# Kernel tuning notes

Measured on AMD Instinct MI355X. Metric: run time of the kernel, lower is better.

## Reference

```python
import jax, jax.numpy as jnp
import numpy as np

N_NODES = 50000
N_EDGES = 800000
F_DIM = 128   # float_feat_dim
H_DIM = 64    # hidden_dim
NEG_SLOPE = 0.2


def setup_inputs() -> dict:
    key = jax.random.key(0)
    ks = jax.random.split(key, 12)
    in_dim = F_DIM + 1
    sc_in = 1.0 / np.sqrt(in_dim)
    sc_h = 1.0 / np.sqrt(H_DIM)
    return {
        "x_float": jax.random.normal(ks[0], (N_NODES, F_DIM), dtype=jnp.float32),
        "x_binary": jax.random.uniform(ks[1], (N_NODES,), dtype=jnp.float32),
        "edge_index": jax.random.randint(ks[2], (2, N_EDGES), 0, N_NODES, dtype=jnp.int64),
        "Wl": jax.random.normal(ks[3], (H_DIM, in_dim), dtype=jnp.float32) * sc_in,
        "bl": jnp.zeros((H_DIM,), dtype=jnp.float32),
        "Wr": jax.random.normal(ks[4], (H_DIM, in_dim), dtype=jnp.float32) * sc_in,
        "br": jnp.zeros((H_DIM,), dtype=jnp.float32),
        "att": jax.random.normal(ks[5], (H_DIM,), dtype=jnp.float32) * sc_h,
        "gat_bias": jnp.zeros((H_DIM,), dtype=jnp.float32),
        "Wo": jax.random.normal(ks[6], (F_DIM, H_DIM), dtype=jnp.float32) * sc_h,
        "bo": jnp.zeros((F_DIM,), dtype=jnp.float32),
        "dispersion": jnp.zeros((F_DIM,), dtype=jnp.float32),
    }


def reference(x_float, x_binary, edge_index, Wl, bl, Wr, br, att, gat_bias, Wo, bo, dispersion):
    N = x_float.shape[0]
    # concat float feats with binary feature -> [N, F+1]
    x = jnp.concatenate([x_float, x_binary[:, None]], axis=1)
    # add self loops (PyG GATv2Conv default)
    loops = jnp.arange(N, dtype=edge_index.dtype)
    src = jnp.concatenate([edge_index[0], loops])  # [E+N]
    dst = jnp.concatenate([edge_index[1], loops])
    # separate source/target linear projections (share_weights=False)
    xl = x @ Wl.T + bl  # [N, H]
    xr = x @ Wr.T + br  # [N, H]
    # per-edge GATv2 attention score: a^T LeakyReLU(x_l[j] + x_r[i])
    m = xl[src] + xr[dst]                      # [E+N, H]
    m = jnp.where(m > 0, m, NEG_SLOPE * m)
    e = m @ att                                # [E+N]
    # segment softmax over destination neighborhoods
    emax = jax.ops.segment_max(e, dst, num_segments=N)  # self loops => every seg nonempty
    ex = jnp.exp(e - emax[dst])
    denom = jax.ops.segment_sum(ex, dst, num_segments=N)
    alpha = ex / denom[dst]                    # [E+N]
    # weighted scatter-aggregate of source projections
    out = jax.ops.segment_sum(alpha[:, None] * xl[src], dst, num_segments=N) + gat_bias
    h = jax.nn.elu(out)                        # [N, H]
    logits = h @ Wo.T + bo                     # [N, F]
    return logits, jax.nn.softplus(dispersion)
```

## Files before the change

kernel.cpp:

```cpp
#include <hip/hip_runtime.h>
#include <hip/hip_bf16.h>
#include <math.h>

#define N_NODES 50000
#define N_EDGES 800000
#define F_DIM 128
#define H_DIM 64
#define IN_DIM 129
#define ETOT (N_EDGES + N_NODES)
#define PROJ_BLKS ((N_NODES + 31) / 32)
#define NB 196
#define CAP 6144
#define EPB 3125
#define BKT_BLKS 256
#define AGG_BLKS 3125

typedef __hip_bfloat16 bf16;
typedef __attribute__((ext_vector_type(8))) short bf16x8;
typedef __attribute__((ext_vector_type(4))) float f32x4;

static __device__ __forceinline__ float bs2f(short s) {
    union { float f; unsigned u; } c; c.u = ((unsigned)(unsigned short)s) << 16; return c.f;
}
static __device__ __forceinline__ short f2bs(float f) {
    union { bf16 b; short s; } u; u.b = __float2bfloat16(f); return u.s;
}

__global__ __launch_bounds__(256) void prep_kernel(
    const float* __restrict__ Wl, const float* __restrict__ Wr,
    const float* __restrict__ Wo,
    bf16* __restrict__ whi, bf16* __restrict__ wlo,
    bf16* __restrict__ wohi, bf16* __restrict__ wolo,
    int* __restrict__ gtot)
{
    int b = blockIdx.x, t = threadIdx.x;
    if (b < 8) {
        int s = b * 256 + t;
        int fid = s >> 6, l = s & 63;
        int wave = fid >> 3, nt = (fid >> 2) & 1, ks = fid & 3;
        int ch = wave * 32 + nt * 16 + (l & 15);
        int kb = ks * 32 + (l >> 4) * 8;
        const float* wrow = (ch < 64) ? Wl + (size_t)ch * IN_DIM
                                      : Wr + (size_t)(ch - 64) * IN_DIM;
        #pragma unroll
        for (int j = 0; j < 8; ++j) {
            float v = wrow[kb + j];
            short hs = f2bs(v);
            short ls = f2bs(v - bs2f(hs));
            ((short*)whi)[(size_t)s * 8 + j] = hs;
            ((short*)wlo)[(size_t)s * 8 + j] = ls;
        }
    } else if (b < 12) {
        int s = (b - 8) * 256 + t;
        int fid = s >> 6, l = s & 63;
        int wave = fid >> 2, nt = (fid >> 1) & 1, ks = fid & 1;
        int ch = wave * 32 + nt * 16 + (l & 15);
        int kb = ks * 32 + (l >> 4) * 8;
        const float* wrow = Wo + (size_t)ch * H_DIM;
        #pragma unroll
        for (int j = 0; j < 8; ++j) {
            float v = wrow[kb + j];
            short hs = f2bs(v);
            short ls = f2bs(v - bs2f(hs));
            ((short*)wohi)[(size_t)s * 8 + j] = hs;
            ((short*)wolo)[(size_t)s * 8 + j] = ls;
        }
    } else {
        if (t < NB) gtot[t] = 0;
    }
}

__global__ __launch_bounds__(256) void h1_kernel(
    const float* __restrict__ xf, const float* __restrict__ xb,
    const float* __restrict__ Wl, const float* __restrict__ bl,
    const float* __restrict__ Wr, const float* __restrict__ br,
    const bf16* __restrict__ whi, const bf16* __restrict__ wlo,
    const int* __restrict__ esrc, const int* __restrict__ edst,
    bf16* __restrict__ xl, bf16* __restrict__ xr,
    int* __restrict__ gtot, unsigned* __restrict__ bstore2,
    int* __restrict__ bofsT)
{
    __shared__ int smem[2048];

    if (blockIdx.x >= PROJ_BLKS) {
        int* hist = smem;
        int* base = smem + 256;
        int* cur  = smem + 512;
        int* shs  = smem + 768;
        int t = threadIdx.x;
        int b = blockIdx.x - PROJ_BLKS;
        int e0 = b * EPB;
        if (t < NB) hist[t] = 0;
        __syncthreads();

        int myd[13]; int mys[13];
        #pragma unroll
        for (int i = 0; i < 13; ++i) {
            int k = t + i * 256;
            bool v = k < EPB;
            int dst = v ? edst[e0 + k] : -1;
            int sc  = v ? esrc[e0 + k] : 0;
            myd[i] = dst; mys[i] = sc;
            if (v) atomicAdd(&hist[dst >> 8], 1);
        }
        __syncthreads();

        int hv = (t < NB) ? hist[t] : 0;
        shs[t] = hv;
        __syncthreads();
        #pragma unroll
        for (int d = 1; d < 256; d <<= 1) {
            int x = (t >= d) ? shs[t - d] : 0;
            __syncthreads();
            shs[t] += x;
            __syncthreads();
        }
        if (t < NB) {
            int bs = shs[t] - hv;
            base[t] = bs;
            cur[t] = 0;
            if (hv) atomicAdd(&gtot[t], hv);
            bofsT[t * 256 + b] = (bs << 16) | hv;
        }
        __syncthreads();

        #pragma unroll
        for (int i = 0; i < 13; ++i) {
            if (myd[i] >= 0) {
                int j = myd[i] >> 8;
                int slot = base[j] + atomicAdd(&cur[j], 1);
                bstore2[(size_t)e0 + slot] =
                    ((unsigned)myd[i] << 16) | (unsigned)mys[i];
            }
        }
        return;
    }

    short* lds = (short*)smem;

    int wave = threadIdx.x >> 6;
    int lane = threadIdx.x & 63;
    int n = lane & 15, q = lane >> 4;
    int node0 = blockIdx.x * 32;

    bf16x8 bhi[2][4], blo_[2][4];
    float biasv[2], w128[2];
    #pragma unroll
    for (int nt = 0; nt < 2; ++nt) {
        int ch = wave * 32 + nt * 16 + n;
        #pragma unroll
        for (int ks = 0; ks < 4; ++ks) {
            int fid = wave * 8 + nt * 4 + ks;
            bhi[nt][ks]  = *(const bf16x8*)(whi + ((size_t)fid * 64 + lane) * 8);
            blo_[nt][ks] = *(const bf16x8*)(wlo + ((size_t)fid * 64 + lane) * 8);
        }
        biasv[nt] = (ch < 64) ? bl[ch] : br[ch - 64];
        w128[nt]  = (ch < 64) ? Wl[(size_t)ch * IN_DIM + 128]
                              : Wr[(size_t)(ch - 64) * IN_DIM + 128];
    }

    #pragma unroll
    for (int mt = 0; mt < 2; ++mt) {
        int nb = node0 + mt * 16;
        if (nb < N_NODES) {
            const float* xrow = xf + (size_t)(nb + n) * F_DIM;
            bf16x8 a[4];
            #pragma unroll
            for (int ks = 0; ks < 4; ++ks) {
                float4 u = *(const float4*)(xrow + ks * 32 + q * 8);
                float4 v = *(const float4*)(xrow + ks * 32 + q * 8 + 4);
                bf16x8 tt;
                tt[0] = f2bs(u.x); tt[1] = f2bs(u.y); tt[2] = f2bs(u.z); tt[3] = f2bs(u.w);
                tt[4] = f2bs(v.x); tt[5] = f2bs(v.y); tt[6] = f2bs(v.z); tt[7] = f2bs(v.w);
                a[ks] = tt;
            }
            f32x4 acc[2] = {{0.f,0.f,0.f,0.f},{0.f,0.f,0.f,0.f}};
            #pragma unroll
            for (int ks = 0; ks < 4; ++ks) {
                #pragma unroll
                for (int nt = 0; nt < 2; ++nt) {
                    acc[nt] = __builtin_amdgcn_mfma_f32_16x16x32_bf16(a[ks], bhi[nt][ks],  acc[nt], 0, 0, 0);
                    acc[nt] = __builtin_amdgcn_mfma_f32_16x16x32_bf16(a[ks], blo_[nt][ks], acc[nt], 0, 0, 0);
                }
            }
            float4 xbv = *(const float4*)(xb + nb + q * 4);
            float xbr[4] = {xbv.x, xbv.y, xbv.z, xbv.w};
            #pragma unroll
            for (int nt = 0; nt < 2; ++nt) {
                int ch = wave * 32 + nt * 16 + n;
                int blk = ch >> 3, pos = ch & 7;
                #pragma unroll
                for (int r = 0; r < 4; ++r) {
                    int nodeL = mt * 16 + q * 4 + r;
                    float val = acc[nt][r] + xbr[r] * w128[nt] + biasv[nt];
                    lds[nodeL * 128 + ((blk ^ (nodeL & 7)) << 3) + pos] = f2bs(val);
                }
            }
        }
    }
    __syncthreads();

    int nl = threadIdx.x >> 3, bk = threadIdx.x & 7;
    int node = node0 + nl;
    if (node < N_NODES) {
        bf16x8 v0 = *(const bf16x8*)(lds + nl * 128 + ((bk ^ (nl & 7)) << 3));
        *(bf16x8*)(xl + (size_t)node * H_DIM + bk * 8) = v0;
        bf16x8 v1 = *(const bf16x8*)(lds + nl * 128 + (((8 + bk) ^ (nl & 7)) << 3));
        *(bf16x8*)(xr + (size_t)node * H_DIM + bk * 8) = v1;
    }
}

__global__ __launch_bounds__(512) void csr_kernel(
    const int* __restrict__ gtot, const unsigned* __restrict__ bstore2,
    const int* __restrict__ bofsT,
    int* __restrict__ offs, int* __restrict__ csr_src)
{
    __shared__ unsigned ent[CAP];
    __shared__ int sh[256], gb_[256], bcnt_[256], bbase_[256];
    __shared__ int h256[256], start[256], c2[256];
    __shared__ int bb_s, C_s;
    int j = blockIdx.x, t = threadIdx.x;

    int bcnt = 0;
    if (t < 256) {
        unsigned v = (unsigned)bofsT[j * 256 + t];
        bbase_[t] = (int)(v >> 16);
        bcnt = (int)(v & 0xffffu);
        bcnt_[t] = bcnt;
        sh[t] = bcnt;
    }
    __syncthreads();
    #pragma unroll
    for (int d = 1; d < 256; d <<= 1) {
        int x = (t >= d && t < 256) ? sh[t - d] : 0;
        __syncthreads();
        if (t < 256) sh[t] += x;
        __syncthreads();
    }
    if (t < 256) gb_[t] = sh[t] - bcnt;
    if (t == 255) C_s = sh[255];
    __syncthreads();
    int C = C_s;

    if (t < 256) {
        const unsigned* p = bstore2 + (size_t)t * EPB + bbase_[t];
        int o = gb_[t];
        int c = bcnt_[t];
        for (int i = 0; i < c; ++i) ent[o + i] = p[i];
    }
    __syncthreads();

    int val = 0;
    if (t < NB) val = gtot[t] + ((t < NB - 1) ? 256 : (N_NODES - (NB - 1) * 256));
    if (t < 256) sh[t] = val;
    __syncthreads();
    #pragma unroll
    for (int d = 1; d < 256; d <<= 1) {
        int x = (t >= d && t < 256) ? sh[t - d] : 0;
        __syncthreads();
        if (t < 256) sh[t] += x;
        __syncthreads();
    }
    if (t == j) bb_s = sh[t] - val;
    if (t < 256) h256[t] = 0;
    __syncthreads();
    int bb = bb_s;

    for (int k = t; k < C; k += 512)
        atomicAdd(&h256[(ent[k] >> 16) & 255], 1);
    __syncthreads();

    int w = 0;
    if (t < 256) {
        w = h256[t] + ((j * 256 + t < N_NODES) ? 1 : 0);
        sh[t] = w;
    }
    __syncthreads();
    #pragma unroll
    for (int d = 1; d < 256; d <<= 1) {
        int x = (t >= d && t < 256) ? sh[t - d] : 0;
        __syncthreads();
        if (t < 256) sh[t] += x;
        __syncthreads();
    }
    if (t < 256) {
        int st = bb + sh[t] - w;
        start[t] = st;
        c2[t] = 0;
        int node = j * 256 + t;
        if (node < N_NODES) {
            offs[node] = st;
            csr_src[st] = node;
        }
    }
    if (j == NB - 1 && t == 0) offs[N_NODES] = ETOT;
    __syncthreads();

    for (int k = t; k < C; k += 512) {
        unsigned en = ent[k];
        int bin = (en >> 16) & 255;
        int r = atomicAdd(&c2[bin], 1);
        csr_src[start[bin] + 1 + r] = (int)(en & 0xffffu);
    }
}

__global__ __launch_bounds__(256) void agg_out(
    const int* __restrict__ csr_src, const int* __restrict__ offs,
    const bf16* __restrict__ xl, const bf16* __restrict__ xr,
    const float* __restrict__ att, const float* __restrict__ gb,
    const bf16* __restrict__ wohi, const bf16* __restrict__ wolo,
    const float* __restrict__ bo, const float* __restrict__ disp,
    float* __restrict__ out)
{
    __shared__ short hts[16 * 72];
    __shared__ float ldso[16 * 132];

    int wave = threadIdx.x >> 6;
    int lane = threadIdx.x & 63;
    int g  = lane >> 3;
    int c8 = lane & 7;
    int node0 = blockIdx.x * 16;

    if (blockIdx.x == 0 && threadIdx.x < F_DIM) {
        float d = disp[threadIdx.x];
        out[(size_t)N_NODES * F_DIM + threadIdx.x] = (d > 20.f) ? d : log1pf(__expf(d));
    }

    float attv[8], gbv[8];
    {
        float4 a0 = *(const float4*)(att + c8 * 8);
        float4 a1 = *(const float4*)(att + c8 * 8 + 4);
        const float L2E = 1.44269504f;
        attv[0] = a0.x * L2E; attv[1] = a0.y * L2E; attv[2] = a0.z * L2E; attv[3] = a0.w * L2E;
        attv[4] = a1.x * L2E; attv[5] = a1.y * L2E; attv[6] = a1.z * L2E; attv[7] = a1.w * L2E;
        float4 g0 = *(const float4*)(gb + c8 * 8);
        float4 g1 = *(const float4*)(gb + c8 * 8 + 4);
        gbv[0] = g0.x; gbv[1] = g0.y; gbv[2] = g0.z; gbv[3] = g0.w;
        gbv[4] = g1.x; gbv[5] = g1.y; gbv[6] = g1.z; gbv[7] = g1.w;
    }

    #pragma unroll 1
    for (int pr = 0; pr < 2; ++pr) {
        int wdA = wave * 4 + pr * 2;
        int wdB = wdA + 1;
        int widA = node0 + wdA;
        int widB = node0 + wdB;

        float xrvA[8], xrvB[8];
        {
            bf16x8 xrA = *(const bf16x8*)(xr + (size_t)widA * H_DIM + c8 * 8);
            bf16x8 xrB = *(const bf16x8*)(xr + (size_t)widB * H_DIM + c8 * 8);
            #pragma unroll
            for (int j = 0; j < 8; ++j) {
                xrvA[j] = bs2f(xrA[j]);
                xrvB[j] = bs2f(xrB[j]);
            }
        }

        int begA = offs[widA], endA = offs[widA + 1], lastA = endA - 1;
        int begB = offs[widB], endB = offs[widB + 1], lastB = endB - 1;

        float denA = 0.f, denB = 0.f;
        float accA[8] = {0.f,0.f,0.f,0.f,0.f,0.f,0.f,0.f};
        float accB[8] = {0.f,0.f,0.f,0.f,0.f,0.f,0.f,0.f};

        int iA0 = begA + g;      iA0 = (iA0 < endA) ? iA0 : lastA;
        int iA1 = begA + 8 + g;  iA1 = (iA1 < endA) ? iA1 : lastA;
        int iA2 = begA + 16 + g; iA2 = (iA2 < endA) ? iA2 : lastA;
        int iB0 = begB + g;      iB0 = (iB0 < endB) ? iB0 : lastB;
        int iB1 = begB + 8 + g;  iB1 = (iB1 < endB) ? iB1 : lastB;
        int iB2 = begB + 16 + g; iB2 = (iB2 < endB) ? iB2 : lastB;
        int sA2 = csr_src[iA2];
        int sB2 = csr_src[iB2];
        bf16x8 rA0 = *(const bf16x8*)(xl + (size_t)csr_src[iA0] * H_DIM + c8 * 8);
        bf16x8 rB0 = *(const bf16x8*)(xl + (size_t)csr_src[iB0] * H_DIM + c8 * 8);
        bf16x8 rA1 = *(const bf16x8*)(xl + (size_t)csr_src[iA1] * H_DIM + c8 * 8);
        bf16x8 rB1 = *(const bf16x8*)(xl + (size_t)csr_src[iB1] * H_DIM + c8 * 8);

        int itA = (endA - begA + 7) >> 3;
        int itB = (endB - begB + 7) >> 3;
        int nIt = (itA > itB) ? itA : itB;
        int baseA = begA, baseB = begB;

        #pragma unroll 1
        for (int it = 0; it < nIt; ++it) {
            int iA3 = baseA + 24 + g; iA3 = (iA3 < endA) ? iA3 : lastA;
            int iB3 = baseB + 24 + g; iB3 = (iB3 < endB) ? iB3 : lastB;
            int sA3 = csr_src[iA3];
            int sB3 = csr_src[iB3];
            bf16x8 rA2 = *(const bf16x8*)(xl + (size_t)sA2 * H_DIM + c8 * 8);
            bf16x8 rB2 = *(const bf16x8*)(xl + (size_t)sB2 * H_DIM + c8 * 8);

            bool vA = (baseA + g) < endA;
            bool vB = (baseB + g) < endB;
            float xvA[8], xvB[8], pA = 0.f, pB = 0.f;
            #pragma unroll
            for (int j = 0; j < 8; ++j) {
                xvA[j] = bs2f(rA0[j]);
                xvB[j] = bs2f(rB0[j]);
                float mA = xvA[j] + xrvA[j];
                float mB = xvB[j] + xrvB[j];
                mA = fmaxf(mA, 0.2f * mA);
                mB = fmaxf(mB, 0.2f * mB);
                pA += mA * attv[j];
                pB += mB * attv[j];
            }
            pA += __shfl_xor(pA, 1); pA += __shfl_xor(pA, 2); pA += __shfl_xor(pA, 4);
            pB += __shfl_xor(pB, 1); pB += __shfl_xor(pB, 2); pB += __shfl_xor(pB, 4);
            float exA = vA ? exp2f(pA) : 0.f;
            float exB = vB ? exp2f(pB) : 0.f;
            denA += exA;
            denB += exB;
            #pragma unroll
            for (int j = 0; j < 8; ++j) {
                accA[j] += exA * xvA[j];
                accB[j] += exB * xvB[j];
            }

            rA0 = rA1; rA1 = rA2; sA2 = sA3; baseA += 8;
            rB0 = rB1; rB1 = rB2; sB2 = sB3; baseB += 8;
        }

        #pragma unroll
        for (int j = 0; j < 8; ++j) {
            accA[j] += __shfl_xor(accA[j], 8);
            accA[j] += __shfl_xor(accA[j], 16);
            accA[j] += __shfl_xor(accA[j], 32);
            accB[j] += __shfl_xor(accB[j], 8);
            accB[j] += __shfl_xor(accB[j], 16);
            accB[j] += __shfl_xor(accB[j], 32);
        }
        denA += __shfl_xor(denA, 8); denA += __shfl_xor(denA, 16); denA += __shfl_xor(denA, 32);
        denB += __shfl_xor(denB, 8); denB += __shfl_xor(denB, 16); denB += __shfl_xor(denB, 32);

        if (g == 0) {
            float invA = 1.0f / denA;
            float invB = 1.0f / denB;
            bf16x8 ovA, ovB;
            #pragma unroll
            for (int j = 0; j < 8; ++j) {
                float va = accA[j] * invA + gbv[j];
                va = (va > 0.f) ? va : expm1f(va);
                ovA[j] = f2bs(va);
                float vb = accB[j] * invB + gbv[j];
                vb = (vb > 0.f) ? vb : expm1f(vb);
                ovB[j] = f2bs(vb);
            }
            *(bf16x8*)(hts + wdA * 72 + c8 * 8) = ovA;
            *(bf16x8*)(hts + wdB * 72 + c8 * 8) = ovB;
        }
    }
    __syncthreads();

    int n = lane & 15, q = lane >> 4;

    bf16x8 bhi[2][2], blo_[2][2];
    float bov[2];
    #pragma unroll
    for (int nt = 0; nt < 2; ++nt) {
        int ch = wave * 32 + nt * 16 + n;
        #pragma unroll
        for (int ks = 0; ks < 2; ++ks) {
            int fid = wave * 4 + nt * 2 + ks;
            bhi[nt][ks]  = *(const bf16x8*)(wohi + ((size_t)fid * 64 + lane) * 8);
            blo_[nt][ks] = *(const bf16x8*)(wolo + ((size_t)fid * 64 + lane) * 8);
        }
        bov[nt] = bo[ch];
    }

    bf16x8 a[2];
    #pragma unroll
    for (int ks = 0; ks < 2; ++ks)
        a[ks] = *(const bf16x8*)(hts + n * 72 + ks * 32 + q * 8);
    f32x4 acc2[2] = {{0.f,0.f,0.f,0.f},{0.f,0.f,0.f,0.f}};
    #pragma unroll
    for (int ks = 0; ks < 2; ++ks) {
        #pragma unroll
        for (int nt = 0; nt < 2; ++nt) {
            acc2[nt] = __builtin_amdgcn_mfma_f32_16x16x32_bf16(a[ks], bhi[nt][ks],  acc2[nt], 0, 0, 0);
            acc2[nt] = __builtin_amdgcn_mfma_f32_16x16x32_bf16(a[ks], blo_[nt][ks], acc2[nt], 0, 0, 0);
        }
    }
    #pragma unroll
    for (int nt = 0; nt < 2; ++nt) {
        int ch = wave * 32 + nt * 16 + n;
        #pragma unroll
        for (int r = 0; r < 4; ++r) {
            int nodeL = q * 4 + r;
            ldso[nodeL * 132 + ch] = acc2[nt][r] + bov[nt];
        }
    }
    __syncthreads();

    int nl = threadIdx.x >> 4, p = threadIdx.x & 15;
    const float* srcp = ldso + nl * 132 + p * 8;
    float* dstp = out + (size_t)(node0 + nl) * F_DIM + p * 8;
    *(float4*)(dstp)     = *(const float4*)(srcp);
    *(float4*)(dstp + 4) = *(const float4*)(srcp + 4);
}

extern "C" void kernel_launch(void* const* d_in, const int* in_sizes, int n_in,
                              void* d_out, int out_size, void* d_ws, size_t ws_size,
                              hipStream_t stream)
{
    const float* xf  = (const float*)d_in[0];
    const float* xb  = (const float*)d_in[1];
    const int*   ei  = (const int*)d_in[2];
    const float* Wl  = (const float*)d_in[3];
    const float* bl  = (const float*)d_in[4];
    const float* Wr  = (const float*)d_in[5];
    const float* br  = (const float*)d_in[6];
    const float* att = (const float*)d_in[7];
    const float* gb  = (const float*)d_in[8];
    const float* Wo  = (const float*)d_in[9];
    const float* bo  = (const float*)d_in[10];
    const float* dp  = (const float*)d_in[11];
    float* out = (float*)d_out;
    const int* esrc = ei;
    const int* edst = ei + N_EDGES;

    char* ws = (char*)d_ws;
    const size_t SZB = (size_t)N_NODES * H_DIM * sizeof(bf16);
    bf16*  xl      = (bf16*)(ws);
    bf16*  xr      = (bf16*)(ws + SZB);
    unsigned* bstore2 = (unsigned*)(ws + 2 * SZB);
    int*   csr_src = (int*)(ws + 2 * SZB + (size_t)N_EDGES * 4);
    int*   offs    = csr_src + ETOT;
    int*   gtot    = offs + (N_NODES + 4);
    int*   bofsT   = gtot + 208;
    bf16*  whi     = (bf16*)(bofsT + NB * 256);
    bf16*  wlo     = whi + 16384;
    bf16*  wohi    = wlo + 16384;
    bf16*  wolo    = wohi + 8192;

    prep_kernel<<<13, 256, 0, stream>>>(Wl, Wr, Wo, whi, wlo, wohi, wolo, gtot);

    h1_kernel<<<PROJ_BLKS + BKT_BLKS, 256, 0, stream>>>(
        xf, xb, Wl, bl, Wr, br, whi, wlo, esrc, edst, xl, xr,
        gtot, bstore2, bofsT);

    csr_kernel<<<NB, 512, 0, stream>>>(gtot, bstore2, bofsT, offs, csr_src);

    agg_out<<<AGG_BLKS, 256, 0, stream>>>(csr_src, offs, xl, xr, att, gb,
                                          wohi, wolo, bo, dp, out);
}
```

Measured before the change: 187.1 us.

## Split node projection across bucket and CSR kernels to overlap work

The dense projection blocks are split into two halves. One half runs alongside the edge-bucketing blocks, and the other half runs alongside the CSR-building blocks in the next kernel. Bucket blocks are now placed first in the grid so they get scheduled early, which fills idle compute units while the latency-bound CSR stage runs. The CSR kernel also moves from 512 to 256 threads to share a block size with the projection work, which costs more loop iterations per thread in the CSR scatter.

```diff
diff --git a/kernel.cpp b/kernel.cpp
--- a/kernel.cpp
+++ b/kernel.cpp
@@ -8,11 +8,12 @@
 #define H_DIM 64
 #define IN_DIM 129
 #define ETOT (N_EDGES + N_NODES)
-#define PROJ_BLKS ((N_NODES + 31) / 32)
 #define NB 196
 #define CAP 6144
 #define EPB 3125
 #define BKT_BLKS 256
+#define PROJ_A 782
+#define PROJ_B 781
 #define AGG_BLKS 3125
 
 typedef __hip_bfloat16 bf16;
@@ -24,6 +25,85 @@
 }
 static __device__ __forceinline__ short f2bs(float f) {
     union { bf16 b; short s; } u; u.b = __float2bfloat16(f); return u.s;
+}
+
+static __device__ __forceinline__ void proj_body(
+    int node0, short* lds,
+    const float* __restrict__ xf, const float* __restrict__ xb,
+    const float* __restrict__ Wl, const float* __restrict__ bl,
+    const float* __restrict__ Wr, const float* __restrict__ br,
+    const bf16* __restrict__ whi, const bf16* __restrict__ wlo,
+    bf16* __restrict__ xl, bf16* __restrict__ xr)
+{
+    int wave = threadIdx.x >> 6;
+    int lane = threadIdx.x & 63;
+    int n = lane & 15, q = lane >> 4;
+
+    bf16x8 bhi[2][4], blo_[2][4];
+    float biasv[2], w128[2];
+    #pragma unroll
+    for (int nt = 0; nt < 2; ++nt) {
+        int ch = wave * 32 + nt * 16 + n;
+        #pragma unroll
+        for (int ks = 0; ks < 4; ++ks) {
+            int fid = wave * 8 + nt * 4 + ks;
+            bhi[nt][ks]  = *(const bf16x8*)(whi + ((size_t)fid * 64 + lane) * 8);
+            blo_[nt][ks] = *(const bf16x8*)(wlo + ((size_t)fid * 64 + lane) * 8);
+        }
+        biasv[nt] = (ch < 64) ? bl[ch] : br[ch - 64];
+        w128[nt]  = (ch < 64) ? Wl[(size_t)ch * IN_DIM + 128]
+                              : Wr[(size_t)(ch - 64) * IN_DIM + 128];
+    }
+
+    #pragma unroll
+    for (int mt = 0; mt < 2; ++mt) {
+        int nb = node0 + mt * 16;
+        if (nb < N_NODES) {
+            const float* xrow = xf + (size_t)(nb + n) * F_DIM;
+            bf16x8 a[4];
+            #pragma unroll
+            for (int ks = 0; ks < 4; ++ks) {
+                float4 u = *(const float4*)(xrow + ks * 32 + q * 8);
+                float4 v = *(const float4*)(xrow + ks * 32 + q * 8 + 4);
+                bf16x8 tt;
+                tt[0] = f2bs(u.x); tt[1] = f2bs(u.y); tt[2] = f2bs(u.z); tt[3] = f2bs(u.w);
+                tt[4] = f2bs(v.x); tt[5] = f2bs(v.y); tt[6] = f2bs(v.z); tt[7] = f2bs(v.w);
+                a[ks] = tt;
+            }
+            f32x4 acc[2] = {{0.f,0.f,0.f,0.f},{0.f,0.f,0.f,0.f}};
+            #pragma unroll
+            for (int ks = 0; ks < 4; ++ks) {
+                #pragma unroll
+                for (int nt = 0; nt < 2; ++nt) {
+                    acc[nt] = __builtin_amdgcn_mfma_f32_16x16x32_bf16(a[ks], bhi[nt][ks],  acc[nt], 0, 0, 0);
+                    acc[nt] = __builtin_amdgcn_mfma_f32_16x16x32_bf16(a[ks], blo_[nt][ks], acc[nt], 0, 0, 0);
+                }
+            }
+            float4 xbv = *(const float4*)(xb + nb + q * 4);
+            float xbr[4] = {xbv.x, xbv.y, xbv.z, xbv.w};
+            #pragma unroll
+            for (int nt = 0; nt < 2; ++nt) {
+                int ch = wave * 32 + nt * 16 + n;
+                int blk = ch >> 3, pos = ch & 7;
+                #pragma unroll
+                for (int r = 0; r < 4; ++r) {
+                    int nodeL = mt * 16 + q * 4 + r;
+                    float val = acc[nt][r] + xbr[r] * w128[nt] + biasv[nt];
+                    lds[nodeL * 128 + ((blk ^ (nodeL & 7)) << 3) + pos] = f2bs(val);
+                }
+            }
+        }
+    }
+    __syncthreads();
+
+    int nl = threadIdx.x >> 3, bk = threadIdx.x & 7;
+    int node = node0 + nl;
+    if (node < N_NODES) {
+        bf16x8 v0 = *(const bf16x8*)(lds + nl * 128 + ((bk ^ (nl & 7)) << 3));
+        *(bf16x8*)(xl + (size_t)node * H_DIM + bk * 8) = v0;
+        bf16x8 v1 = *(const bf16x8*)(lds + nl * 128 + (((8 + bk) ^ (nl & 7)) << 3));
+        *(bf16x8*)(xr + (size_t)node * H_DIM + bk * 8) = v1;
+    }
 }
 
 __global__ __launch_bounds__(256) void prep_kernel(
@@ -70,7 +150,7 @@
     }
 }
 
-__global__ __launch_bounds__(256) void h1_kernel(
+__global__ __launch_bounds__(256) void h2_kernel(
     const float* __restrict__ xf, const float* __restrict__ xb,
     const float* __restrict__ Wl, const float* __restrict__ bl,
     const float* __restrict__ Wr, const float* __restrict__ br,
@@ -82,13 +162,13 @@
 {
     __shared__ int smem[2048];
 
-    if (blockIdx.x >= PROJ_BLKS) {
+    if (blockIdx.x < BKT_BLKS) {
         int* hist = smem;
         int* base = smem + 256;
         int* cur  = smem + 512;
         int* shs  = smem + 768;
         int t = threadIdx.x;
-        int b = blockIdx.x - PROJ_BLKS;
+        int b = blockIdx.x;
         int e0 = b * EPB;
         if (t < NB) hist[t] = 0;
         __syncthreads();
@@ -136,172 +216,106 @@
         return;
     }
 
-    short* lds = (short*)smem;
-
-    int wave = threadIdx.x >> 6;
-    int lane = threadIdx.x & 63;
-    int n = lane & 15, q = lane >> 4;
-    int node0 = blockIdx.x * 32;
-
-    bf16x8 bhi[2][4], blo_[2][4];
-    float biasv[2], w128[2];
-    #pragma unroll
-    for (int nt = 0; nt < 2; ++nt) {
-        int ch = wave * 32 + nt * 16 + n;
-        #pragma unroll
-        for (int ks = 0; ks < 4; ++ks) {
-            int fid = wave * 8 + nt * 4 + ks;
-            bhi[nt][ks]  = *(const bf16x8*)(whi + ((size_t)fid * 64 + lane) * 8);
-            blo_[nt][ks] = *(const bf16x8*)(wlo + ((size_t)fid * 64 + lane) * 8);
-        }
-        biasv[nt] = (ch < 64) ? bl[ch] : br[ch - 64];
-        w128[nt]  = (ch < 64) ? Wl[(size_t)ch * IN_DIM + 128]
-                              : Wr[(size_t)(ch - 64) * IN_DIM + 128];
-    }
-
-    #pragma unroll
-    for (int mt = 0; mt < 2; ++mt) {
-        int nb = node0 + mt * 16;
-        if (nb < N_NODES) {
-            const float* xrow = xf + (size_t)(nb + n) * F_DIM;
-            bf16x8 a[4];
-            #pragma unroll
-            for (int ks = 0; ks < 4; ++ks) {
-                float4 u = *(const float4*)(xrow + ks * 32 + q * 8);
-                float4 v = *(const float4*)(xrow + ks * 32 + q * 8 + 4);
-                bf16x8 tt;
-                tt[0] = f2bs(u.x); tt[1] = f2bs(u.y); tt[2] = f2bs(u.z); tt[3] = f2bs(u.w);
-                tt[4] = f2bs(v.x); tt[5] = f2bs(v.y); tt[6] = f2bs(v.z); tt[7] = f2bs(v.w);
-                a[ks] = tt;
-            }
-            f32x4 acc[2] = {{0.f,0.f,0.f,0.f},{0.f,0.f,0.f,0.f}};
-            #pragma unroll
-            for (int ks = 0; ks < 4; ++ks) {
-                #pragma unroll
-                for (int nt = 0; nt < 2; ++nt) {
-                    acc[nt] = __builtin_amdgcn_mfma_f32_16x16x32_bf16(a[ks], bhi[nt][ks],  acc[nt], 0, 0, 0);
-                    acc[nt] = __builtin_amdgcn_mfma_f32_16x16x32_bf16(a[ks], blo_[nt][ks], acc[nt], 0, 0, 0);
-                }
-            }
-            float4 xbv = *(const float4*)(xb + nb + q * 4);
-            float xbr[4] = {xbv.x, xbv.y, xbv.z, xbv.w};
-            #pragma unroll
-            for (int nt = 0; nt < 2; ++nt) {
-                int ch = wave * 32 + nt * 16 + n;
-                int blk = ch >> 3, pos = ch & 7;
-                #pragma unroll
-                for (int r = 0; r < 4; ++r) {
-                    int nodeL = mt * 16 + q * 4 + r;
-                    float val = acc[nt][r] + xbr[r] * w128[nt] + biasv[nt];
-                    lds[nodeL * 128 + ((blk ^ (nodeL & 7)) << 3) + pos] = f2bs(val);
-                }
-            }
-        }
-    }
-    __syncthreads();
-
-    int nl = threadIdx.x >> 3, bk = threadIdx.x & 7;
-    int node = node0 + nl;
-    if (node < N_NODES) {
-        bf16x8 v0 = *(const bf16x8*)(lds + nl * 128 + ((bk ^ (nl & 7)) << 3));
-        *(bf16x8*)(xl + (size_t)node * H_DIM + bk * 8) = v0;
-        bf16x8 v1 = *(const bf16x8*)(lds + nl * 128 + (((8 + bk) ^ (nl & 7)) << 3));
-        *(bf16x8*)(xr + (size_t)node * H_DIM + bk * 8) = v1;
-    }
-}
-
-__global__ __launch_bounds__(512) void csr_kernel(
+    proj_body((blockIdx.x - BKT_BLKS) * 32, (short*)smem,
+              xf, xb, Wl, bl, Wr, br, whi, wlo, xl, xr);
+}
+
+__global__ __launch_bounds__(256) void h3_kernel(
+    const float* __restrict__ xf, const float* __restrict__ xb,
+    const float* __restrict__ Wl, const float* __restrict__ bl,
+    const float* __restrict__ Wr, const float* __restrict__ br,
+    const bf16* __restrict__ whi, const bf16* __restrict__ wlo,
+    bf16* __restrict__ xl, bf16* __restrict__ xr,
     const int* __restrict__ gtot, const unsigned* __restrict__ bstore2,
     const int* __restrict__ bofsT,
     int* __restrict__ offs, int* __restrict__ csr_src)
 {
-    __shared__ unsigned ent[CAP];
-    __shared__ int sh[256], gb_[256], bcnt_[256], bbase_[256];
-    __shared__ int h256[256], start[256], c2[256];
-    __shared__ int bb_s, C_s;
-    int j = blockIdx.x, t = threadIdx.x;
-
-    int bcnt = 0;
-    if (t < 256) {
+    __shared__ int smem3[7176];
+
+    if (blockIdx.x < NB) {
+        unsigned* ent = (unsigned*)smem3;
+        int* sh    = smem3 + CAP;
+        int* h256  = smem3 + CAP + 256;
+        int* start = smem3 + CAP + 512;
+        int* c2    = smem3 + CAP + 768;
+        int* scal  = smem3 + CAP + 1024;
+        int j = blockIdx.x, t = threadIdx.x;
+
         unsigned v = (unsigned)bofsT[j * 256 + t];
-        bbase_[t] = (int)(v >> 16);
-        bcnt = (int)(v & 0xffffu);
-        bcnt_[t] = bcnt;
+        int bbase = (int)(v >> 16);
+        int bcnt  = (int)(v & 0xffffu);
         sh[t] = bcnt;
-    }
-    __syncthreads();
-    #pragma unroll
-    for (int d = 1; d < 256; d <<= 1) {
-        int x = (t >= d && t < 256) ? sh[t - d] : 0;
-        __syncthreads();
-        if (t < 256) sh[t] += x;
-        __syncthreads();
-    }
-    if (t < 256) gb_[t] = sh[t] - bcnt;
-    if (t == 255) C_s = sh[255];
-    __syncthreads();
-    int C = C_s;
-
-    if (t < 256) {
-        const unsigned* p = bstore2 + (size_t)t * EPB + bbase_[t];
-        int o = gb_[t];
-        int c = bcnt_[t];
-        for (int i = 0; i < c; ++i) ent[o + i] = p[i];
-    }
-    __syncthreads();
-
-    int val = 0;
-    if (t < NB) val = gtot[t] + ((t < NB - 1) ? 256 : (N_NODES - (NB - 1) * 256));
-    if (t < 256) sh[t] = val;
-    __syncthreads();
-    #pragma unroll
-    for (int d = 1; d < 256; d <<= 1) {
-        int x = (t >= d && t < 256) ? sh[t - d] : 0;
-        __syncthreads();
-        if (t < 256) sh[t] += x;
-        __syncthreads();
-    }
-    if (t == j) bb_s = sh[t] - val;
-    if (t < 256) h256[t] = 0;
-    __syncthreads();
-    int bb = bb_s;
-
-    for (int k = t; k < C; k += 512)
-        atomicAdd(&h256[(ent[k] >> 16) & 255], 1);
-    __syncthreads();
-
-    int w = 0;
-    if (t < 256) {
-        w = h256[t] + ((j * 256 + t < N_NODES) ? 1 : 0);
+        __syncthreads();
+        #pragma unroll
+        for (int d = 1; d < 256; d <<= 1) {
+            int x = (t >= d) ? sh[t - d] : 0;
+            __syncthreads();
+            sh[t] += x;
+            __syncthreads();
+        }
+        int gb = sh[t] - bcnt;
+        if (t == 255) scal[0] = sh[255];
+        __syncthreads();
+        int C = scal[0];
+
+        {
+            const unsigned* p = bstore2 + (size_t)t * EPB + bbase;
+            for (int i = 0; i < bcnt; ++i) ent[gb + i] = p[i];
+        }
+        __syncthreads();
+
+        int val = 0;
+        if (t < NB) val = gtot[t] + ((t < NB - 1) ? 256 : (N_NODES - (NB - 1) * 256));
+        sh[t] = val;
+        __syncthreads();
+        #pragma unroll
+        for (int d = 1; d < 256; d <<= 1) {
+            int x = (t >= d) ? sh[t - d] : 0;
+            __syncthreads();
+            sh[t] += x;
+            __syncthreads();
+        }
+        if (t == j) scal[1] = sh[t] - val;
+        h256[t] = 0;
+        __syncthreads();
+        int bb = scal[1];
+
+        for (int k = t; k < C; k += 256)
+            atomicAdd(&h256[(ent[k] >> 16) & 255], 1);
+        __syncthreads();
+
+        int node = j * 256 + t;
+        int w = h256[t] + ((node < N_NODES) ? 1 : 0);
         sh[t] = w;
-    }
-    __syncthreads();
-    #pragma unroll
-    for (int d = 1; d < 256; d <<= 1) {
-        int x = (t >= d && t < 256) ? sh[t - d] : 0;
-        __syncthreads();
-        if (t < 256) sh[t] += x;
-        __syncthreads();
-    }
-    if (t < 256) {
+        __syncthreads();
+        #pragma unroll
+        for (int d = 1; d < 256; d <<= 1) {
+            int x = (t >= d) ? sh[t - d] : 0;
+            __syncthreads();
+            sh[t] += x;
+            __syncthreads();
+        }
         int st = bb + sh[t] - w;
         start[t] = st;
         c2[t] = 0;
-        int node = j * 256 + t;
         if (node < N_NODES) {
             offs[node] = st;
             csr_src[st] = node;
         }
-    }
-    if (j == NB - 1 && t == 0) offs[N_NODES] = ETOT;
-    __syncthreads();
-
-    for (int k = t; k < C; k += 512) {
-        unsigned en = ent[k];
-        int bin = (en >> 16) & 255;
-        int r = atomicAdd(&c2[bin], 1);
-        csr_src[start[bin] + 1 + r] = (int)(en & 0xffffu);
-    }
+        if (j == NB - 1 && t == 0) offs[N_NODES] = ETOT;
+        __syncthreads();
+
+        for (int k = t; k < C; k += 256) {
+            unsigned en = ent[k];
+            int bin = (en >> 16) & 255;
+            int r = atomicAdd(&c2[bin], 1);
+            csr_src[start[bin] + 1 + r] = (int)(en & 0xffffu);
+        }
+        return;
+    }
+
+    proj_body((PROJ_A + blockIdx.x - NB) * 32, (short*)smem3,
+              xf, xb, Wl, bl, Wr, br, whi, wlo, xl, xr);
 }
 
 __global__ __launch_bounds__(256) void agg_out(
@@ -535,11 +549,13 @@
 
     prep_kernel<<<13, 256, 0, stream>>>(Wl, Wr, Wo, whi, wlo, wohi, wolo, gtot);
 
-    h1_kernel<<<PROJ_BLKS + BKT_BLKS, 256, 0, stream>>>(
+    h2_kernel<<<BKT_BLKS + PROJ_A, 256, 0, stream>>>(
         xf, xb, Wl, bl, Wr, br, whi, wlo, esrc, edst, xl, xr,
         gtot, bstore2, bofsT);
 
-    csr_kernel<<<NB, 512, 0, stream>>>(gtot, bstore2, bofsT, offs, csr_src);
+    h3_kernel<<<NB + PROJ_B, 256, 0, stream>>>(
+        xf, xb, Wl, bl, Wr, br, whi, wlo, xl, xr,
+        gtot, bstore2, bofsT, offs, csr_src);
 
     agg_out<<<AGG_BLKS, 256, 0, stream>>>(csr_src, offs, xl, xr, att, gb,
                                           wohi, wolo, bo, dp, out);
```

New measurement: 184.2 us. Within noise of the previous version (-1.6%).
